# Kernel tuning notes

Hardware: AMD Instinct MI355X
Metric: run time of the kernel (lower is better)

## Reference

```python
import jax, jax.numpy as jnp
import numpy as np

B, N, M, C, H = 4, 8192, 8192, 512, 8
D = C // H  # head_dim = 64

def setup_inputs() -> dict:
    key = jax.random.key(0)
    ks = jax.random.split(key, 10)
    s = 1.0 / np.sqrt(C)
    return {
        "x": jax.random.normal(ks[0], (B, N, C), dtype=jnp.float32),
        "y": jax.random.normal(ks[1], (B, M, C), dtype=jnp.float32),
        "Wq": jax.random.normal(ks[2], (C, C), dtype=jnp.float32) * s,
        "bq": jax.random.normal(ks[3], (C,), dtype=jnp.float32) * s,
        "Wk": jax.random.normal(ks[4], (C, C), dtype=jnp.float32) * s,
        "bk": jax.random.normal(ks[5], (C,), dtype=jnp.float32) * s,
        "Wv": jax.random.normal(ks[6], (C, C), dtype=jnp.float32) * s,
        "bv": jax.random.normal(ks[7], (C,), dtype=jnp.float32) * s,
        "Wp": jax.random.normal(ks[8], (C, C), dtype=jnp.float32) * s,
        "bp": jax.random.normal(ks[9], (C,), dtype=jnp.float32) * s,
    }

def reference(x, y, Wq, bq, Wk, bk, Wv, bv, Wp, bp):
    # project and split heads: (B, S, C) -> (B, H, S, D)
    def heads(t, W, b, S):
        return (t @ W + b).reshape(B, S, H, D).transpose(0, 2, 1, 3)
    q = jax.nn.softmax(heads(x, Wq, bq, N), axis=-1)   # (B,H,N,D)
    k = jax.nn.softmax(heads(y, Wk, bk, M), axis=-1)   # (B,H,M,D)
    v = heads(y, Wv, bv, M)                             # (B,H,M,D)
    # denom: (q * sum_m k).sum_d, clamped
    ksum = jnp.sum(k, axis=2, keepdims=True)            # (B,H,1,D)
    denom = jnp.maximum(jnp.sum(q * ksum, axis=-1, keepdims=True), 1e-6)  # (B,H,N,1)
    # reassociated k^T @ v: (B,H,D,D), then q @ (k^T v)
    kv = jnp.einsum("bhmd,bhme->bhde", k, v)
    out = jnp.einsum("bhnd,bhde->bhne", q, kv) / denom + q  # (B,H,N,D)
    out = out.transpose(0, 2, 1, 3).reshape(B, N, C)
    return out @ Wp + bp  # dropout rate 0.0 -> identity
```

## Files before the change

kernel.cpp:

```cpp
#include <hip/hip_runtime.h>

typedef __bf16 bf16_t;
typedef __bf16 bf16x4 __attribute__((ext_vector_type(4)));
typedef __bf16 bf16x8 __attribute__((ext_vector_type(8)));
typedef float f32x4 __attribute__((ext_vector_type(4)));

#define AS1 __attribute__((address_space(1)))
#define AS3 __attribute__((address_space(3)))

__device__ __forceinline__ void gll16(const void* g, void* l) {
  __builtin_amdgcn_global_load_lds((AS1 void*)g, (AS3 void*)l, 16, 0, 0);
}

template <int ACT>
__launch_bounds__(256, 2)
__global__ void gemm_k(const bf16_t* __restrict__ A, const bf16_t* __restrict__ BT,
                       const float* __restrict__ bias, void* __restrict__ Cout) {
  __shared__ __align__(16) bf16_t As[128 * 64];
  __shared__ __align__(16) bf16_t Bs[128 * 64];
  const int tid = threadIdx.x;
  const int lane = tid & 63, wid = tid >> 6;
  const int wr = wid >> 1, wc = wid & 1;
  const int rowbase = blockIdx.x * 128, colbase = blockIdx.y * 128;

  f32x4 zero = {0.f, 0.f, 0.f, 0.f};
  f32x4 acc[4][4];
#pragma unroll
  for (int i = 0; i < 4; ++i)
#pragma unroll
    for (int j = 0; j < 4; ++j) acc[i][j] = zero;

  const int srow = wid * 8 + (lane >> 3);
  const int scol = (lane & 7) * 8;
  const size_t abase = (size_t)(rowbase + srow) * 512 + scol;
  const size_t bbase = (size_t)(colbase + srow) * 512 + scol;
  bf16_t* lA = As + wid * 512;
  bf16_t* lB = Bs + wid * 512;

  for (int k0 = 0; k0 < 512; k0 += 64) {
#pragma unroll
    for (int i = 0; i < 4; ++i) {
      gll16(A + abase + (size_t)i * (32 * 512) + k0, lA + i * 2048);
      gll16(BT + bbase + (size_t)i * (32 * 512) + k0, lB + i * 2048);
    }
    __syncthreads();
#pragma unroll
    for (int kk = 0; kk < 64; kk += 32) {
      bf16x8 af[4], bfr[4];
#pragma unroll
      for (int ri = 0; ri < 4; ++ri)
        af[ri] = *(const bf16x8*)&As[(wr * 64 + ri * 16 + (lane & 15)) * 64 + kk + (lane >> 4) * 8];
#pragma unroll
      for (int ci = 0; ci < 4; ++ci)
        bfr[ci] = *(const bf16x8*)&Bs[(wc * 64 + ci * 16 + (lane & 15)) * 64 + kk + (lane >> 4) * 8];
#pragma unroll
      for (int ri = 0; ri < 4; ++ri)
#pragma unroll
        for (int ci = 0; ci < 4; ++ci)
          acc[ri][ci] = __builtin_amdgcn_mfma_f32_16x16x32_bf16(af[ri], bfr[ci], acc[ri][ci], 0, 0, 0);
    }
    __syncthreads();
  }

  float bb[4];
#pragma unroll
  for (int ci = 0; ci < 4; ++ci) bb[ci] = bias[colbase + wc * 64 + ci * 16 + (lane & 15)];
#pragma unroll
  for (int ri = 0; ri < 4; ++ri)
#pragma unroll
    for (int ci = 0; ci < 4; ++ci)
#pragma unroll
      for (int r = 0; r < 4; ++r) acc[ri][ci][r] += bb[ci];

  if (ACT == 1) {
#pragma unroll
    for (int ri = 0; ri < 4; ++ri) {
#pragma unroll
      for (int r = 0; r < 4; ++r) {
        float m = fmaxf(fmaxf(acc[ri][0][r], acc[ri][1][r]), fmaxf(acc[ri][2][r], acc[ri][3][r]));
        m = fmaxf(m, __shfl_xor(m, 1));
        m = fmaxf(m, __shfl_xor(m, 2));
        m = fmaxf(m, __shfl_xor(m, 4));
        m = fmaxf(m, __shfl_xor(m, 8));
        float s = 0.f;
#pragma unroll
        for (int ci = 0; ci < 4; ++ci) {
          float p = __expf(acc[ri][ci][r] - m);
          acc[ri][ci][r] = p;
          s += p;
        }
        s += __shfl_xor(s, 1);
        s += __shfl_xor(s, 2);
        s += __shfl_xor(s, 4);
        s += __shfl_xor(s, 8);
        float rcp = 1.0f / s;
#pragma unroll
        for (int ci = 0; ci < 4; ++ci) acc[ri][ci][r] *= rcp;
      }
    }
  }

  const int lr = (lane >> 4) * 4, lc = lane & 15;
#pragma unroll
  for (int ri = 0; ri < 4; ++ri)
#pragma unroll
    for (int ci = 0; ci < 4; ++ci)
#pragma unroll
      for (int r = 0; r < 4; ++r) {
        size_t idx = (size_t)(rowbase + wr * 64 + ri * 16 + lr + r) * 512 +
                     (colbase + wc * 64 + ci * 16 + lc);
        if (ACT == 2)
          ((float*)Cout)[idx] = acc[ri][ci][r];
        else
          ((bf16_t*)Cout)[idx] = (bf16_t)acc[ri][ci][r];
      }
}

__launch_bounds__(256)
__global__ void kv_k(const bf16_t* __restrict__ K, const bf16_t* __restrict__ V,
                     float* __restrict__ kv, float* __restrict__ ksum) {
  __shared__ __align__(16) bf16_t Ks[128 * 64];
  __shared__ __align__(16) bf16_t Vs[128 * 64];
  const int SPLIT = 16;
  const int bh = blockIdx.x / SPLIT, sp = blockIdx.x % SPLIT;
  const int b = bh >> 3, h = bh & 7;
  const int tid = threadIdx.x;
  const int d0 = (tid >> 4) * 4, e0 = (tid & 15) * 4;
  float acc[4][4] = {{0.f}};
  float ks[4] = {0.f, 0.f, 0.f, 0.f};

  for (int c = 0; c < 4; ++c) {
    const int m0 = sp * 512 + c * 128;
#pragma unroll
    for (int i = 0; i < 4; ++i) {
      int f = i * 2048 + tid * 8;
      int row = f >> 6, col = f & 63;
      size_t g = (size_t)(b * 8192 + m0 + row) * 512 + h * 64 + col;
      *(int4*)&Ks[f] = *(const int4*)&K[g];
      *(int4*)&Vs[f] = *(const int4*)&V[g];
    }
    __syncthreads();
    for (int m = 0; m < 128; ++m) {
      bf16x4 kb = *(const bf16x4*)&Ks[m * 64 + d0];
      bf16x4 vb = *(const bf16x4*)&Vs[m * 64 + e0];
      float kx[4], vx[4];
#pragma unroll
      for (int a = 0; a < 4; ++a) {
        kx[a] = (float)kb[a];
        vx[a] = (float)vb[a];
      }
#pragma unroll
      for (int a = 0; a < 4; ++a)
#pragma unroll
        for (int e = 0; e < 4; ++e) acc[a][e] += kx[a] * vx[e];
      if ((tid & 15) == 0) {
#pragma unroll
        for (int a = 0; a < 4; ++a) ks[a] += kx[a];
      }
    }
    __syncthreads();
  }
#pragma unroll
  for (int a = 0; a < 4; ++a)
#pragma unroll
    for (int e = 0; e < 4; ++e)
      atomicAdd(&kv[(size_t)(bh * 64 + d0 + a) * 64 + e0 + e], acc[a][e]);
  if ((tid & 15) == 0) {
#pragma unroll
    for (int a = 0; a < 4; ++a) atomicAdd(&ksum[bh * 64 + d0 + a], ks[a]);
  }
}

__global__ void build_kvB(const float* __restrict__ kv, const float* __restrict__ ksum,
                          bf16_t* __restrict__ kvB) {
  int i = blockIdx.x * 256 + threadIdx.x;
  if (i >= 32 * 80 * 64) return;
  int k = i & 63;
  int col = (i >> 6) % 80;
  int bh = i / (80 * 64);
  float v = 0.f;
  if (col < 64)
    v = kv[(size_t)(bh * 64 + k) * 64 + col];
  else if (col == 64)
    v = ksum[bh * 64 + k];
  kvB[i] = (bf16_t)v;
}

__launch_bounds__(256, 2)
__global__ void attn_k(const bf16_t* __restrict__ Q, const bf16_t* __restrict__ kvB,
                       bf16_t* __restrict__ attn) {
  __shared__ __align__(16) bf16_t As[128 * 64];
  const int rt = blockIdx.x;
  const int h = blockIdx.y;
  const int b = rt >> 6;
  const int bh = b * 8 + h;
  const int tid = threadIdx.x, lane = tid & 63, wid = tid >> 6;
  const int srow = wid * 8 + (lane >> 3);
  const int scol = (lane & 7) * 8;
#pragma unroll
  for (int i = 0; i < 4; ++i)
    gll16(Q + (size_t)(rt * 128 + srow + i * 32) * 512 + h * 64 + scol, As + wid * 512 + i * 2048);

  f32x4 zero = {0.f, 0.f, 0.f, 0.f};
  f32x4 acc[2][5];
#pragma unroll
  for (int i = 0; i < 2; ++i)
#pragma unroll
    for (int j = 0; j < 5; ++j) acc[i][j] = zero;
  __syncthreads();

  const bf16_t* Bb = kvB + (size_t)bh * (80 * 64);
#pragma unroll
  for (int kk = 0; kk < 64; kk += 32) {
    bf16x8 af[2];
#pragma unroll
    for (int ri = 0; ri < 2; ++ri)
      af[ri] = *(const bf16x8*)&As[(wid * 32 + ri * 16 + (lane & 15)) * 64 + kk + (lane >> 4) * 8];
#pragma unroll
    for (int ci = 0; ci < 5; ++ci) {
      bf16x8 bfr = *(const bf16x8*)&Bb[(ci * 16 + (lane & 15)) * 64 + kk + (lane >> 4) * 8];
#pragma unroll
      for (int ri = 0; ri < 2; ++ri)
        acc[ri][ci] = __builtin_amdgcn_mfma_f32_16x16x32_bf16(af[ri], bfr, acc[ri][ci], 0, 0, 0);
    }
  }

  const int lr = (lane >> 4) * 4, lc = lane & 15;
#pragma unroll
  for (int ri = 0; ri < 2; ++ri)
#pragma unroll
    for (int r = 0; r < 4; ++r) {
      float dn = __shfl(acc[ri][4][r], lane & 48);
      dn = fmaxf(dn, 1e-6f);
      float rinv = 1.0f / dn;
      int rl = wid * 32 + ri * 16 + lr + r;
#pragma unroll
      for (int ci = 0; ci < 4; ++ci) {
        int e = ci * 16 + lc;
        float qv = (float)As[rl * 64 + e];
        float o = acc[ri][ci][r] * rinv + qv;
        attn[(size_t)(rt * 128 + rl) * 512 + h * 64 + e] = (bf16_t)o;
      }
    }
}

__global__ void cvt_k(const float* __restrict__ in, bf16_t* __restrict__ out, int n4) {
  int i = blockIdx.x * blockDim.x + threadIdx.x;
  if (i < n4) {
    float4 v = ((const float4*)in)[i];
    bf16x4 o;
    o[0] = (bf16_t)v.x;
    o[1] = (bf16_t)v.y;
    o[2] = (bf16_t)v.z;
    o[3] = (bf16_t)v.w;
    ((bf16x4*)out)[i] = o;
  }
}

__global__ void wtrans_k(const float* __restrict__ W, bf16_t* __restrict__ WT) {
  int i = blockIdx.x * 256 + threadIdx.x;
  int n = i >> 9, k = i & 511;
  WT[i] = (bf16_t)W[k * 512 + n];
}

__global__ void zero_k(float* __restrict__ p, int n) {
  int i = blockIdx.x * 256 + threadIdx.x;
  if (i < n) p[i] = 0.f;
}

extern "C" void kernel_launch(void* const* d_in, const int* in_sizes, int n_in,
                              void* d_out, int out_size, void* d_ws, size_t ws_size,
                              hipStream_t stream) {
  (void)in_sizes; (void)n_in; (void)out_size; (void)ws_size;
  const float* x  = (const float*)d_in[0];
  const float* y  = (const float*)d_in[1];
  const float* Wq = (const float*)d_in[2];
  const float* bq = (const float*)d_in[3];
  const float* Wk = (const float*)d_in[4];
  const float* bk = (const float*)d_in[5];
  const float* Wv = (const float*)d_in[6];
  const float* bv = (const float*)d_in[7];
  const float* Wp = (const float*)d_in[8];
  const float* bp = (const float*)d_in[9];
  float* out = (float*)d_out;

  char* ws = (char*)d_ws;
  const size_t MB = 1024 * 1024;
  bf16_t* xbf = (bf16_t*)(ws + 0);
  bf16_t* ybf = (bf16_t*)(ws + 32 * MB);
  bf16_t* Qb  = (bf16_t*)(ws + 64 * MB);
  bf16_t* Kb  = (bf16_t*)(ws + 96 * MB);
  bf16_t* Vb  = (bf16_t*)(ws + 128 * MB);
  bf16_t* WqT = (bf16_t*)(ws + 160 * MB);
  bf16_t* WkT = WqT + 512 * 512;
  bf16_t* WvT = WkT + 512 * 512;
  bf16_t* WpT = WvT + 512 * 512;
  float* kv   = (float*)(ws + 163 * MB);
  float* ksum = kv + 32 * 64 * 64;
  bf16_t* kvB = (bf16_t*)(ws + 164 * MB);
  bf16_t* attn = xbf;

  cvt_k<<<16384, 256, 0, stream>>>(x, xbf, 4194304);
  cvt_k<<<16384, 256, 0, stream>>>(y, ybf, 4194304);
  wtrans_k<<<1024, 256, 0, stream>>>(Wq, WqT);
  wtrans_k<<<1024, 256, 0, stream>>>(Wk, WkT);
  wtrans_k<<<1024, 256, 0, stream>>>(Wv, WvT);
  wtrans_k<<<1024, 256, 0, stream>>>(Wp, WpT);

  dim3 gg(256, 4);
  gemm_k<1><<<gg, 256, 0, stream>>>(xbf, WqT, bq, Qb);
  gemm_k<1><<<gg, 256, 0, stream>>>(ybf, WkT, bk, Kb);
  gemm_k<0><<<gg, 256, 0, stream>>>(ybf, WvT, bv, Vb);

  zero_k<<<(133120 + 255) / 256, 256, 0, stream>>>(kv, 133120);
  kv_k<<<512, 256, 0, stream>>>(Kb, Vb, kv, ksum);
  build_kvB<<<(32 * 80 * 64) / 256, 256, 0, stream>>>(kv, ksum, kvB);

  attn_k<<<dim3(256, 8), 256, 0, stream>>>(Qb, kvB, attn);

  gemm_k<2><<<gg, 256, 0, stream>>>(attn, WpT, bp, out);
}
```

Baseline: 399.5 us.

## Compute K^T V with MFMA using transposed K/V layout from projection GEMMs

```diff
diff --git a/kernel.cpp b/kernel.cpp
--- a/kernel.cpp
+++ b/kernel.cpp
@@ -12,7 +12,7 @@
   __builtin_amdgcn_global_load_lds((AS1 void*)g, (AS3 void*)l, 16, 0, 0);
 }
 
-template <int ACT>
+template <int ACT, bool TRANS>
 __launch_bounds__(256, 2)
 __global__ void gemm_k(const bf16_t* __restrict__ A, const bf16_t* __restrict__ BT,
                        const float* __restrict__ bias, void* __restrict__ Cout) {
@@ -107,67 +107,81 @@
     for (int ci = 0; ci < 4; ++ci)
 #pragma unroll
       for (int r = 0; r < 4; ++r) {
-        size_t idx = (size_t)(rowbase + wr * 64 + ri * 16 + lr + r) * 512 +
-                     (colbase + wc * 64 + ci * 16 + lc);
-        if (ACT == 2)
-          ((float*)Cout)[idx] = acc[ri][ci][r];
-        else
+        int gm = rowbase + wr * 64 + ri * 16 + lr + r;
+        int c = colbase + wc * 64 + ci * 16 + lc;
+        if (TRANS) {
+          size_t idx = ((size_t)((gm >> 13) * 8 + (c >> 6)) * 64 + (c & 63)) * 8192 + (gm & 8191);
           ((bf16_t*)Cout)[idx] = (bf16_t)acc[ri][ci][r];
+        } else {
+          size_t idx = (size_t)gm * 512 + c;
+          if (ACT == 2)
+            ((float*)Cout)[idx] = acc[ri][ci][r];
+          else
+            ((bf16_t*)Cout)[idx] = (bf16_t)acc[ri][ci][r];
+        }
       }
 }
 
-__launch_bounds__(256)
-__global__ void kv_k(const bf16_t* __restrict__ K, const bf16_t* __restrict__ V,
-                     float* __restrict__ kv, float* __restrict__ ksum) {
-  __shared__ __align__(16) bf16_t Ks[128 * 64];
-  __shared__ __align__(16) bf16_t Vs[128 * 64];
-  const int SPLIT = 16;
-  const int bh = blockIdx.x / SPLIT, sp = blockIdx.x % SPLIT;
-  const int b = bh >> 3, h = bh & 7;
-  const int tid = threadIdx.x;
-  const int d0 = (tid >> 4) * 4, e0 = (tid & 15) * 4;
-  float acc[4][4] = {{0.f}};
-  float ks[4] = {0.f, 0.f, 0.f, 0.f};
-
-  for (int c = 0; c < 4; ++c) {
-    const int m0 = sp * 512 + c * 128;
-#pragma unroll
-    for (int i = 0; i < 4; ++i) {
-      int f = i * 2048 + tid * 8;
-      int row = f >> 6, col = f & 63;
-      size_t g = (size_t)(b * 8192 + m0 + row) * 512 + h * 64 + col;
-      *(int4*)&Ks[f] = *(const int4*)&K[g];
-      *(int4*)&Vs[f] = *(const int4*)&V[g];
+__launch_bounds__(256, 2)
+__global__ void kv2_k(const bf16_t* __restrict__ Kt, const bf16_t* __restrict__ Vt,
+                      float* __restrict__ kv, float* __restrict__ ksum) {
+  __shared__ __align__(16) bf16_t Ks[64 * 64];
+  __shared__ __align__(16) bf16_t Vs[64 * 64];
+  const int bh = blockIdx.x >> 4, sp = blockIdx.x & 15;
+  const int tid = threadIdx.x, lane = tid & 63, wid = tid >> 6;
+  const size_t base = (size_t)bh * 64 * 8192;
+  const int m0 = sp * 512;
+  const int srow = wid * 8 + (lane >> 3);
+  const int scol = (lane & 7) * 8;
+
+  f32x4 zero = {0.f, 0.f, 0.f, 0.f};
+  f32x4 acc[4], accs[4];
+#pragma unroll
+  for (int i = 0; i < 4; ++i) { acc[i] = zero; accs[i] = zero; }
+  bf16x8 ones;
+#pragma unroll
+  for (int j = 0; j < 8; ++j) ones[j] = (bf16_t)1.0f;
+
+  for (int c = 0; c < 8; ++c) {
+    const int mc = m0 + c * 64;
+#pragma unroll
+    for (int i = 0; i < 2; ++i) {
+      size_t g = base + (size_t)(srow + i * 32) * 8192 + mc + scol;
+      gll16(Kt + g, Ks + wid * 512 + i * 2048);
+      gll16(Vt + g, Vs + wid * 512 + i * 2048);
     }
     __syncthreads();
-    for (int m = 0; m < 128; ++m) {
-      bf16x4 kb = *(const bf16x4*)&Ks[m * 64 + d0];
-      bf16x4 vb = *(const bf16x4*)&Vs[m * 64 + e0];
-      float kx[4], vx[4];
-#pragma unroll
-      for (int a = 0; a < 4; ++a) {
-        kx[a] = (float)kb[a];
-        vx[a] = (float)vb[a];
+#pragma unroll
+    for (int kk = 0; kk < 64; kk += 32) {
+      bf16x8 af[4];
+#pragma unroll
+      for (int ri = 0; ri < 4; ++ri)
+        af[ri] = *(const bf16x8*)&Ks[(ri * 16 + (lane & 15)) * 64 + kk + (lane >> 4) * 8];
+      bf16x8 bfr = *(const bf16x8*)&Vs[(wid * 16 + (lane & 15)) * 64 + kk + (lane >> 4) * 8];
+#pragma unroll
+      for (int ri = 0; ri < 4; ++ri)
+        acc[ri] = __builtin_amdgcn_mfma_f32_16x16x32_bf16(af[ri], bfr, acc[ri], 0, 0, 0);
+      if (wid == 0) {
+#pragma unroll
+        for (int ri = 0; ri < 4; ++ri)
+          accs[ri] = __builtin_amdgcn_mfma_f32_16x16x32_bf16(af[ri], ones, accs[ri], 0, 0, 0);
       }
-#pragma unroll
-      for (int a = 0; a < 4; ++a)
-#pragma unroll
-        for (int e = 0; e < 4; ++e) acc[a][e] += kx[a] * vx[e];
-      if ((tid & 15) == 0) {
-#pragma unroll
-        for (int a = 0; a < 4; ++a) ks[a] += kx[a];
-      }
     }
     __syncthreads();
   }
-#pragma unroll
-  for (int a = 0; a < 4; ++a)
-#pragma unroll
-    for (int e = 0; e < 4; ++e)
-      atomicAdd(&kv[(size_t)(bh * 64 + d0 + a) * 64 + e0 + e], acc[a][e]);
-  if ((tid & 15) == 0) {
-#pragma unroll
-    for (int a = 0; a < 4; ++a) atomicAdd(&ksum[bh * 64 + d0 + a], ks[a]);
+
+  const int lr = (lane >> 4) * 4, lc = lane & 15;
+#pragma unroll
+  for (int ri = 0; ri < 4; ++ri)
+#pragma unroll
+    for (int r = 0; r < 4; ++r)
+      atomicAdd(&kv[((size_t)bh * 64 + ri * 16 + lr + r) * 64 + wid * 16 + lc], acc[ri][r]);
+  if (wid == 0 && lc == 0) {
+#pragma unroll
+    for (int ri = 0; ri < 4; ++ri)
+#pragma unroll
+      for (int r = 0; r < 4; ++r)
+        atomicAdd(&ksum[bh * 64 + ri * 16 + lr + r], accs[ri][r]);
   }
 }
 
@@ -289,8 +303,8 @@
   bf16_t* xbf = (bf16_t*)(ws + 0);
   bf16_t* ybf = (bf16_t*)(ws + 32 * MB);
   bf16_t* Qb  = (bf16_t*)(ws + 64 * MB);
-  bf16_t* Kb  = (bf16_t*)(ws + 96 * MB);
-  bf16_t* Vb  = (bf16_t*)(ws + 128 * MB);
+  bf16_t* Kt  = (bf16_t*)(ws + 96 * MB);
+  bf16_t* Vt  = (bf16_t*)(ws + 128 * MB);
   bf16_t* WqT = (bf16_t*)(ws + 160 * MB);
   bf16_t* WkT = WqT + 512 * 512;
   bf16_t* WvT = WkT + 512 * 512;
@@ -308,15 +322,15 @@
   wtrans_k<<<1024, 256, 0, stream>>>(Wp, WpT);
 
   dim3 gg(256, 4);
-  gemm_k<1><<<gg, 256, 0, stream>>>(xbf, WqT, bq, Qb);
-  gemm_k<1><<<gg, 256, 0, stream>>>(ybf, WkT, bk, Kb);
-  gemm_k<0><<<gg, 256, 0, stream>>>(ybf, WvT, bv, Vb);
+  gemm_k<1, false><<<gg, 256, 0, stream>>>(xbf, WqT, bq, Qb);
+  gemm_k<1, true><<<gg, 256, 0, stream>>>(ybf, WkT, bk, Kt);
+  gemm_k<0, true><<<gg, 256, 0, stream>>>(ybf, WvT, bv, Vt);
 
   zero_k<<<(133120 + 255) / 256, 256, 0, stream>>>(kv, 133120);
-  kv_k<<<512, 256, 0, stream>>>(Kb, Vb, kv, ksum);
+  kv2_k<<<512, 256, 0, stream>>>(Kt, Vt, kv, ksum);
   build_kvB<<<(32 * 80 * 64) / 256, 256, 0, stream>>>(kv, ksum, kvB);
 
   attn_k<<<dim3(256, 8), 256, 0, stream>>>(Qb, kvB, attn);
 
-  gemm_k<2><<<gg, 256, 0, stream>>>(attn, WpT, bp, out);
-}
+  gemm_k<2, false><<<gg, 256, 0, stream>>>(attn, WpT, bp, out);
+}
```

After: 357.3 us. -10.6%, faster.
